# Kernel tuning notes

Measured on AMD Instinct MI355X. Metric: run time of the kernel, lower is better.

The kernel has to match this reference:

```python
import jax, jax.numpy as jnp
import numpy as np

N, DIM, HEADS, DHEAD = 4096, 1024, 16, 64
INNER = HEADS * DHEAD


def setup_inputs() -> dict:
    key = jax.random.key(0)
    ks = jax.random.split(key, 6)
    s_in = 1.0 / np.sqrt(DIM)
    s_inner = 1.0 / np.sqrt(INNER)
    return {
        "x": jax.random.normal(ks[0], (N, DIM), dtype=jnp.float32),
        # weights stored as (in, out) so y = x @ W
        "Wq": jax.random.uniform(ks[1], (DIM, INNER), jnp.float32, -s_in, s_in),
        "Wk": jax.random.uniform(ks[2], (DIM, INNER), jnp.float32, -s_in, s_in),
        "Wv": jax.random.uniform(ks[3], (DIM, INNER), jnp.float32, -s_in, s_in),
        "Wo": jax.random.uniform(ks[4], (INNER, DIM), jnp.float32, -s_inner, s_inner),
        "bo": jax.random.uniform(ks[5], (DIM,), jnp.float32, -s_inner, s_inner),
    }


def reference(x, Wq, Wk, Wv, Wo, bo):
    scale = DHEAD ** -0.5
    # [n, h, d] -> [h, n, d]
    q = (x @ Wq).reshape(N, HEADS, DHEAD).transpose(1, 0, 2)
    k = (x @ Wk).reshape(N, HEADS, DHEAD).transpose(1, 0, 2)
    v = (x @ Wv).reshape(N, HEADS, DHEAD).transpose(1, 0, 2)
    dots = jnp.einsum("hnd,hmd->hnm", q, k) * scale  # [h, n, n]
    attn = jax.nn.softmax(dots, axis=-1)
    out = jnp.einsum("hnm,hmd->hnd", attn, v)  # [h, n, d]
    out = out.transpose(1, 0, 2).reshape(N, INNER)
    return out @ Wo + bo
```

## Files before the change

### kernel.cpp

```cpp
#include <hip/hip_runtime.h>
#include <cstdint>
#include <cstddef>

typedef _Float16 f16;
typedef _Float16 f16x8 __attribute__((ext_vector_type(8)));
typedef _Float16 f16x4 __attribute__((ext_vector_type(4)));
typedef __fp16 fp16x2 __attribute__((ext_vector_type(2)));
typedef float floatx4 __attribute__((ext_vector_type(4)));
typedef float floatx16 __attribute__((ext_vector_type(16)));

constexpr int SEQ = 4096;
constexpr int DIM = 1024;
constexpr int NHEAD = 16;
constexpr int DH = 64;

#define QSCALE 0.18033688011112042f

__device__ __forceinline__ void async16(void* lds, const void* g) {
  __builtin_amdgcn_global_load_lds(
      (__attribute__((address_space(1))) void*)g,
      (__attribute__((address_space(3))) void*)lds, 16, 0, 0);
}

__device__ __forceinline__ uint32_t pk2(float a, float b) {
  union { fp16x2 h; uint32_t u; } c;
  c.h = __builtin_amdgcn_cvt_pkrtz(a, b);
  return c.u;
}

__device__ __forceinline__ float dot2acc(uint32_t packed, float acc) {
#if __has_builtin(__builtin_amdgcn_fdot2)
  union { uint32_t u; fp16x2 h; } c; c.u = packed;
  fp16x2 one2; one2.x = (__fp16)1.0f; one2.y = (__fp16)1.0f;
  return __builtin_amdgcn_fdot2(c.h, one2, acc, false);
#else
  union { uint32_t u; fp16x2 h; } c; c.u = packed;
  return acc + (float)c.h.x + (float)c.h.y;
#endif
}


__global__ void cvt_x(const float* __restrict__ x, f16* __restrict__ xh) {
  int i = (blockIdx.x * 256 + threadIdx.x) * 4;
  float4 v = *(const float4*)(x + i);
  f16x4 o;
  o.x = (f16)v.x; o.y = (f16)v.y; o.z = (f16)v.z; o.w = (f16)v.w;
  *(f16x4*)(xh + i) = o;
}

__global__ void transpose_cvt(const float* __restrict__ w0, const float* __restrict__ w1,
                              const float* __restrict__ w2, const float* __restrict__ w3,
                              f16* __restrict__ o0, f16* __restrict__ o1,
                              f16* __restrict__ o2, f16* __restrict__ o3) {
  __shared__ float tile[32][33];
  int z = blockIdx.z;
  const float* W = (z == 0) ? w0 : (z == 1) ? w1 : (z == 2) ? w2 : w3;
  f16* O = (z == 0) ? o0 : (z == 1) ? o1 : (z == 2) ? o2 : o3;
  int tx = threadIdx.x, ty = threadIdx.y;
  int xc = blockIdx.x * 32 + tx;
  for (int i = ty; i < 32; i += 8)
    tile[i][tx] = W[(size_t)(blockIdx.y * 32 + i) * DIM + xc];
  __syncthreads();
  int xo = blockIdx.y * 32 + tx;
  for (int i = ty; i < 32; i += 8)
    O[(size_t)(blockIdx.x * 32 + i) * DIM + xo] = (f16)tile[tx][i];
}

__global__ __launch_bounds__(256, 3) void gemm_qkv(
    const f16* __restrict__ xh, const f16* __restrict__ wqt,
    const f16* __restrict__ wkt, const f16* __restrict__ wvt,
    f16* __restrict__ q_ws, f16* __restrict__ k_ws, f16* __restrict__ vt_ws) {
  __shared__ f16 smem[16896];
  f16* a_lds = smem;
  f16* b_lds = smem + 4096;
  const int tid = threadIdx.x;
  const int lane = tid & 63, l16 = lane & 15, quad = lane >> 4;
  const int w = tid >> 6, wr = w >> 1, wc = w & 1;
  const int m0 = blockIdx.x * 128, n0 = blockIdx.y * 128;
  const int z = blockIdx.z;
  const f16* Bt = (z == 0) ? wqt : (z == 1) ? wkt : wvt;

  floatx4 acc[4][4];
#pragma unroll
  for (int mt = 0; mt < 4; ++mt)
#pragma unroll
    for (int nt = 0; nt < 4; ++nt) acc[mt][nt] = (floatx4){0.f, 0.f, 0.f, 0.f};

  for (int k0 = 0; k0 < DIM; k0 += 32) {
#pragma unroll
    for (int rnd = 0; rnd < 2; ++rnd) {
      int e = (rnd * 256 + tid) * 8;
      int cb = e >> 10, r = (e >> 3) & 127;
      async16(a_lds + e, xh + (size_t)(m0 + r) * DIM + k0 + cb * 8);
      async16(b_lds + e, Bt + (size_t)(n0 + r) * DIM + k0 + cb * 8);
    }
    __syncthreads();
    f16x8 af[4], bq[4];
#pragma unroll
    for (int mt = 0; mt < 4; ++mt)
      af[mt] = *(const f16x8*)(a_lds + quad * 1024 + (wr * 64 + mt * 16 + l16) * 8);
#pragma unroll
    for (int nt = 0; nt < 4; ++nt)
      bq[nt] = *(const f16x8*)(b_lds + quad * 1024 + (wc * 64 + nt * 16 + l16) * 8);
#pragma unroll
    for (int mt = 0; mt < 4; ++mt)
#pragma unroll
      for (int nt = 0; nt < 4; ++nt)
        acc[mt][nt] = __builtin_amdgcn_mfma_f32_16x16x32_f16(af[mt], bq[nt], acc[mt][nt], 0, 0, 0);
    __syncthreads();
  }

  if (z < 2) {
#pragma unroll
    for (int mt = 0; mt < 4; ++mt)
#pragma unroll
      for (int nt = 0; nt < 4; ++nt)
#pragma unroll
        for (int r = 0; r < 4; ++r) {
          int m = m0 + wr * 64 + mt * 16 + quad * 4 + r;
          int c = n0 + wc * 64 + nt * 16 + l16;
          float v = acc[mt][nt][r];
          if (z == 0)
            q_ws[(size_t)((c >> 6) * SEQ + m) * DH + (c & 63)] = (f16)(v * QSCALE);
          else
            k_ws[(size_t)((c >> 6) * SEQ + m) * DH + (c & 63)] = (f16)v;
        }
  } else {
#pragma unroll
    for (int mt = 0; mt < 4; ++mt)
#pragma unroll
      for (int nt = 0; nt < 4; ++nt)
#pragma unroll
        for (int r = 0; r < 4; ++r) {
          int cl = wc * 64 + nt * 16 + l16;
          int ml = wr * 64 + mt * 16 + quad * 4 + r;
          smem[cl * 132 + ml] = (f16)acc[mt][nt][r];
        }
    __syncthreads();
#pragma unroll
    for (int it = 0; it < 8; ++it) {
      int idx = it * 256 + tid;
      int cl = idx >> 4, mp = (idx & 15) * 8;
      f16x4 lo = *(const f16x4*)(smem + cl * 132 + mp);
      f16x4 hi4 = *(const f16x4*)(smem + cl * 132 + mp + 4);
      f16x8 v8;
#pragma unroll
      for (int j = 0; j < 4; ++j) { v8[j] = lo[j]; v8[4 + j] = hi4[j]; }
      *(f16x8*)(vt_ws + (size_t)(n0 + cl) * SEQ + m0 + mp) = v8;
    }
  }
}

__global__ __launch_bounds__(256, 4) void attn_kernel(
    const f16* __restrict__ qg, const f16* __restrict__ kg,
    const f16* __restrict__ vtg, f16* __restrict__ po, float* __restrict__ ps) {
  __shared__ f16 smem[16384];
  f16* k_lds = smem;
  f16* v_lds = smem + 8192;

  const int tid = threadIdx.x;
  const int w = tid >> 6, lane = tid & 63, l32 = lane & 31;
  const int hi = lane >> 5;
  const int h = blockIdx.y, qt = blockIdx.x, half = blockIdx.z;
  const int q0 = qt * 128 + w * 32;

  f16x8 qf[4];
#pragma unroll
  for (int kf = 0; kf < 4; ++kf)
    qf[kf] = *(const f16x8*)(qg + (size_t)(h * SEQ + q0 + l32) * DH + kf * 16 + hi * 8);

  floatx16 oacc[2];
  oacc[0] = (floatx16)0.f; oacc[1] = (floatx16)0.f;
  float ssum = 0.f;

  const int kt0 = half * (SEQ / 256), kt1 = kt0 + (SEQ / 256);
  for (int kt = kt0; kt < kt1; ++kt) {
#pragma unroll
    for (int rnd = 0; rnd < 4; ++rnd) {
      int e = (rnd * 256 + tid) * 8;
      {
        int cb = e >> 10, r = (e >> 3) & 127;
        async16(k_lds + e, kg + (size_t)(h * SEQ + kt * 128 + r) * DH + cb * 8);
      }
      {
        int cb = e >> 9, r = (e >> 3) & 63;
        async16(v_lds + e, vtg + (size_t)(h * DH + r) * SEQ + kt * 128 + cb * 8);
      }
    }
    __syncthreads();

#pragma unroll
    for (int kb = 0; kb < 4; ++kb) {
      floatx16 sacc = (floatx16)0.f;
#pragma unroll
      for (int kf = 0; kf < 4; ++kf) {
        f16x8 kfrag = *(const f16x8*)(k_lds + (kf * 2 + hi) * 1024 + (kb * 32 + l32) * 8);
        sacc = __builtin_amdgcn_mfma_f32_32x32x16_f16(kfrag, qf[kf], sacc, 0, 0, 0);
      }
      float p[16];
#pragma unroll
      for (int r = 0; r < 16; ++r) p[r] = exp2f(sacc[r]);
#pragma unroll
      for (int kh = 0; kh < 2; ++kh) {
        uint32_t d0a = pk2(p[8 * kh + 0], p[8 * kh + 1]);
        uint32_t d0b = pk2(p[8 * kh + 2], p[8 * kh + 3]);
        uint32_t d1a = pk2(p[8 * kh + 4], p[8 * kh + 5]);
        uint32_t d1b = pk2(p[8 * kh + 6], p[8 * kh + 7]);
        ssum = dot2acc(d0a, ssum);
        ssum = dot2acc(d0b, ssum);
        ssum = dot2acc(d1a, ssum);
        ssum = dot2acc(d1b, ssum);
        uint32_t ra = (uint32_t)__shfl_xor((int)(hi ? d0a : d1a), 32);
        uint32_t rb = (uint32_t)__shfl_xor((int)(hi ? d0b : d1b), 32);
        union { uint32_t u[4]; f16x8 v; } bu;
        bu.u[0] = hi ? ra : d0a;
        bu.u[1] = hi ? rb : d0b;
        bu.u[2] = hi ? d1a : ra;
        bu.u[3] = hi ? d1b : rb;
        f16x8 bfrag = bu.v;
        int cb = kb * 4 + kh * 2 + hi;
#pragma unroll
        for (int dt = 0; dt < 2; ++dt) {
          f16x8 vfrag = *(const f16x8*)(v_lds + cb * 512 + (dt * 32 + l32) * 8);
          oacc[dt] = __builtin_amdgcn_mfma_f32_32x32x16_f16(vfrag, bfrag, oacc[dt], 0, 0, 0);
        }
      }
    }
    __syncthreads();
  }

  ssum += __shfl_xor(ssum, 32);
  const int tileid = (half * NHEAD + h) * 32 + qt;
  if (hi == 0) ps[(size_t)tileid * 128 + w * 32 + l32] = ssum;

  f16* pob = po + (size_t)tileid * 8192;
#pragma unroll
  for (int dt = 0; dt < 2; ++dt)
#pragma unroll
    for (int r = 0; r < 16; ++r) {
      int d = dt * 32 + (r & 3) + 8 * (r >> 2) + 4 * hi;
      pob[d * 128 + w * 32 + l32] = (f16)oacc[dt][r];
    }
}

__global__ __launch_bounds__(256, 4) void combine(
    const f16* __restrict__ po, const float* __restrict__ ps, f16* __restrict__ og) {
  __shared__ float inv_s[128];
  __shared__ f16 t[128 * 68];
  const int tid = threadIdx.x;
  const int h = blockIdx.y, qt = blockIdx.x;
  const int t0 = h * 32 + qt, t1 = (NHEAD + h) * 32 + qt;
  if (tid < 128) inv_s[tid] = 1.f / (ps[(size_t)t0 * 128 + tid] + ps[(size_t)t1 * 128 + tid]);
  __syncthreads();
  const f16* b0 = po + (size_t)t0 * 8192;
  const f16* b1 = po + (size_t)t1 * 8192;
#pragma unroll
  for (int it = 0; it < 4; ++it) {
    int e = (it * 256 + tid) * 8;
    int d = e >> 7, q = e & 127;
    f16x8 a = *(const f16x8*)(b0 + e);
    f16x8 b = *(const f16x8*)(b1 + e);
#pragma unroll
    for (int j = 0; j < 8; ++j)
      t[(q + j) * 68 + d] = (f16)(((float)a[j] + (float)b[j]) * inv_s[q + j]);
  }
  __syncthreads();
#pragma unroll
  for (int it = 0; it < 4; ++it) {
    int idx = it * 256 + tid;
    int q = idx >> 3, dcol = (idx & 7) * 8;
    f16x4 lo = *(const f16x4*)(t + q * 68 + dcol);
    f16x4 hi4 = *(const f16x4*)(t + q * 68 + dcol + 4);
    f16x8 v8;
#pragma unroll
    for (int j = 0; j < 4; ++j) { v8[j] = lo[j]; v8[4 + j] = hi4[j]; }
    *(f16x8*)(og + (size_t)(qt * 128 + q) * DIM + h * DH + dcol) = v8;
  }
}

__global__ __launch_bounds__(256, 2) void gemm_o(
    const f16* __restrict__ ab, const f16* __restrict__ wot,
    const float* __restrict__ bo, float* __restrict__ out) {
  __shared__ f16 a_lds[4096];
  __shared__ f16 b_lds[2048];
  const int tid = threadIdx.x;
  const int lane = tid & 63, l16 = lane & 15, quad = lane >> 4;
  const int w = tid >> 6, wr = w >> 1, wc = w & 1;
  const int m0 = blockIdx.x * 128, n0 = blockIdx.y * 64;

  floatx4 acc[4][2];
#pragma unroll
  for (int mt = 0; mt < 4; ++mt)
#pragma unroll
    for (int nt = 0; nt < 2; ++nt) acc[mt][nt] = (floatx4){0.f, 0.f, 0.f, 0.f};

  for (int k0 = 0; k0 < DIM; k0 += 32) {
#pragma unroll
    for (int rnd = 0; rnd < 2; ++rnd) {
      int e = (rnd * 256 + tid) * 8;
      int cb = e >> 10, r = (e >> 3) & 127;
      async16(a_lds + e, ab + (size_t)(m0 + r) * DIM + k0 + cb * 8);
    }
    {
      int e = tid * 8;
      int cb = e >> 9, r = (e >> 3) & 63;
      async16(b_lds + e, wot + (size_t)(n0 + r) * DIM + k0 + cb * 8);
    }
    __syncthreads();
    f16x8 af[4], bq[2];
#pragma unroll
    for (int mt = 0; mt < 4; ++mt)
      af[mt] = *(const f16x8*)(a_lds + quad * 1024 + (wr * 64 + mt * 16 + l16) * 8);
#pragma unroll
    for (int nt = 0; nt < 2; ++nt)
      bq[nt] = *(const f16x8*)(b_lds + quad * 512 + (wc * 32 + nt * 16 + l16) * 8);
#pragma unroll
    for (int mt = 0; mt < 4; ++mt)
#pragma unroll
      for (int nt = 0; nt < 2; ++nt)
        acc[mt][nt] = __builtin_amdgcn_mfma_f32_16x16x32_f16(af[mt], bq[nt], acc[mt][nt], 0, 0, 0);
    __syncthreads();
  }

#pragma unroll
  for (int mt = 0; mt < 4; ++mt)
#pragma unroll
    for (int nt = 0; nt < 2; ++nt)
#pragma unroll
      for (int r = 0; r < 4; ++r) {
        int m = m0 + wr * 64 + mt * 16 + quad * 4 + r;
        int c = n0 + wc * 32 + nt * 16 + l16;
        out[(size_t)m * DIM + c] = acc[mt][nt][r] + bo[c];
      }
}


extern "C" void kernel_launch(void* const* d_in, const int* in_sizes, int n_in,
                              void* d_out, int out_size, void* d_ws, size_t ws_size,
                              hipStream_t stream) {
  (void)in_sizes; (void)n_in; (void)out_size; (void)ws_size;
  const float* x  = (const float*)d_in[0];
  const float* Wq = (const float*)d_in[1];
  const float* Wk = (const float*)d_in[2];
  const float* Wv = (const float*)d_in[3];
  const float* Wo = (const float*)d_in[4];
  const float* bo = (const float*)d_in[5];
  float* out = (float*)d_out;
  char* ws = (char*)d_ws;

  f16* xh    = (f16*)(ws);
  f16* wqt   = (f16*)(ws + (8u  << 20));
  f16* wkt   = (f16*)(ws + (10u << 20));
  f16* wvt   = (f16*)(ws + (12u << 20));
  f16* wot   = (f16*)(ws + (14u << 20));
  f16* q_ws  = (f16*)(ws + (16u << 20));
  f16* k_ws  = (f16*)(ws + (24u << 20));
  f16* vt_ws = (f16*)(ws + (32u << 20));
  f16* po    = (f16*)(ws + (40u << 20));
  float* ps  = (float*)(ws + (57u << 20));
  f16* aout  = xh;

  cvt_x<<<dim3(SEQ * DIM / 1024), dim3(256), 0, stream>>>(x, xh);
  transpose_cvt<<<dim3(32, 32, 4), dim3(32, 8), 0, stream>>>(Wq, Wk, Wv, Wo, wqt, wkt, wvt, wot);
  gemm_qkv<<<dim3(32, 8, 3), dim3(256), 0, stream>>>(xh, wqt, wkt, wvt, q_ws, k_ws, vt_ws);
  attn_kernel<<<dim3(SEQ / 128, NHEAD, 2), dim3(256), 0, stream>>>(q_ws, k_ws, vt_ws, po, ps);
  combine<<<dim3(SEQ / 128, NHEAD), dim3(256), 0, stream>>>(po, ps, aout);
  gemm_o<<<dim3(32, 16), dim3(256), 0, stream>>>(aout, wot, bo, out);
}
```

Measured before the change: 292.1 us.

## Double-buffer K/V tiles in attention with async prefetch and permlane swap

The attention loop now uses a two-stage LDS ping-pong with 64-key tiles. The next tile's K and V^T are prefetched via async global-to-LDS loads while the current tile is computed, and the kernel waits with explicit vmcnt counts and raw s_barrier instead of __syncthreads. It also replaces the cross-half shuffle with permlane32_swap when available and raises wave priority around MFMA groups. The goal is to hide global load latency behind compute, at the cost of more barriers per key (smaller tiles) and a hand-written waitcnt that must match the issue count.

```diff
diff --git a/kernel.cpp b/kernel.cpp
--- a/kernel.cpp
+++ b/kernel.cpp
@@ -155,8 +155,6 @@
     const f16* __restrict__ qg, const f16* __restrict__ kg,
     const f16* __restrict__ vtg, f16* __restrict__ po, float* __restrict__ ps) {
   __shared__ f16 smem[16384];
-  f16* k_lds = smem;
-  f16* v_lds = smem + 8192;
 
   const int tid = threadIdx.x;
   const int w = tid >> 6, lane = tid & 63, l32 = lane & 31;
@@ -173,30 +171,54 @@
   oacc[0] = (floatx16)0.f; oacc[1] = (floatx16)0.f;
   float ssum = 0.f;
 
-  const int kt0 = half * (SEQ / 256), kt1 = kt0 + (SEQ / 256);
-  for (int kt = kt0; kt < kt1; ++kt) {
-#pragma unroll
-    for (int rnd = 0; rnd < 4; ++rnd) {
+  const f16* kg_h = kg + (size_t)h * SEQ * DH;
+  const f16* vt_h = vtg + (size_t)h * DH * SEQ;
+  const int kb0 = half * (SEQ / 128);
+  constexpr int NT = SEQ / 128;
+
+  {
+    const f16* ks = kg_h + (size_t)(kb0 * 64) * DH;
+    const f16* vs = vt_h + kb0 * 64;
+#pragma unroll
+    for (int rnd = 0; rnd < 2; ++rnd) {
       int e = (rnd * 256 + tid) * 8;
-      {
-        int cb = e >> 10, r = (e >> 3) & 127;
-        async16(k_lds + e, kg + (size_t)(h * SEQ + kt * 128 + r) * DH + cb * 8);
+      int cb = e >> 9, r = (e >> 3) & 63;
+      async16(smem + e, ks + (size_t)r * DH + cb * 8);
+      async16(smem + 4096 + e, vs + (size_t)r * SEQ + cb * 8);
+    }
+  }
+
+  for (int i = 0; i < NT; ++i) {
+    f16* k_lds = smem + (i & 1) * 8192;
+    f16* v_lds = k_lds + 4096;
+    if (i + 1 < NT) {
+      f16* kn = smem + ((i + 1) & 1) * 8192;
+      const f16* ks = kg_h + (size_t)((kb0 + i + 1) * 64) * DH;
+      const f16* vs = vt_h + (kb0 + i + 1) * 64;
+#pragma unroll
+      for (int rnd = 0; rnd < 2; ++rnd) {
+        int e = (rnd * 256 + tid) * 8;
+        int cb = e >> 9, r = (e >> 3) & 63;
+        async16(kn + e, ks + (size_t)r * DH + cb * 8);
+        async16(kn + 4096 + e, vs + (size_t)r * SEQ + cb * 8);
       }
-      {
-        int cb = e >> 9, r = (e >> 3) & 63;
-        async16(v_lds + e, vtg + (size_t)(h * DH + r) * SEQ + kt * 128 + cb * 8);
-      }
-    }
-    __syncthreads();
-
-#pragma unroll
-    for (int kb = 0; kb < 4; ++kb) {
+      asm volatile("s_waitcnt vmcnt(4)" ::: "memory");
+    } else {
+      asm volatile("s_waitcnt vmcnt(0)" ::: "memory");
+    }
+    __builtin_amdgcn_s_barrier();
+    asm volatile("" ::: "memory");
+
+#pragma unroll
+    for (int kb = 0; kb < 2; ++kb) {
       floatx16 sacc = (floatx16)0.f;
+      __builtin_amdgcn_s_setprio(1);
 #pragma unroll
       for (int kf = 0; kf < 4; ++kf) {
-        f16x8 kfrag = *(const f16x8*)(k_lds + (kf * 2 + hi) * 1024 + (kb * 32 + l32) * 8);
+        f16x8 kfrag = *(const f16x8*)(k_lds + (kf * 2 + hi) * 512 + (kb * 32 + l32) * 8);
         sacc = __builtin_amdgcn_mfma_f32_32x32x16_f16(kfrag, qf[kf], sacc, 0, 0, 0);
       }
+      __builtin_amdgcn_s_setprio(0);
       float p[16];
 #pragma unroll
       for (int r = 0; r < 16; ++r) p[r] = exp2f(sacc[r]);
@@ -210,23 +232,36 @@
         ssum = dot2acc(d0b, ssum);
         ssum = dot2acc(d1a, ssum);
         ssum = dot2acc(d1b, ssum);
-        uint32_t ra = (uint32_t)__shfl_xor((int)(hi ? d0a : d1a), 32);
-        uint32_t rb = (uint32_t)__shfl_xor((int)(hi ? d0b : d1b), 32);
         union { uint32_t u[4]; f16x8 v; } bu;
-        bu.u[0] = hi ? ra : d0a;
-        bu.u[1] = hi ? rb : d0b;
-        bu.u[2] = hi ? d1a : ra;
-        bu.u[3] = hi ? d1b : rb;
-        f16x8 bfrag = bu.v;
+#if __has_builtin(__builtin_amdgcn_permlane32_swap)
+        {
+          auto s1 = __builtin_amdgcn_permlane32_swap(d0a, d1a, false, false);
+          auto s2 = __builtin_amdgcn_permlane32_swap(d0b, d1b, false, false);
+          bu.u[0] = s1[0]; bu.u[1] = s2[0]; bu.u[2] = s1[1]; bu.u[3] = s2[1];
+        }
+#else
+        {
+          uint32_t ra = (uint32_t)__shfl_xor((int)(hi ? d0a : d1a), 32);
+          uint32_t rb = (uint32_t)__shfl_xor((int)(hi ? d0b : d1b), 32);
+          bu.u[0] = hi ? ra : d0a;
+          bu.u[1] = hi ? rb : d0b;
+          bu.u[2] = hi ? d1a : ra;
+          bu.u[3] = hi ? d1b : rb;
+        }
+#endif
         int cb = kb * 4 + kh * 2 + hi;
+        __builtin_amdgcn_s_setprio(1);
 #pragma unroll
         for (int dt = 0; dt < 2; ++dt) {
           f16x8 vfrag = *(const f16x8*)(v_lds + cb * 512 + (dt * 32 + l32) * 8);
-          oacc[dt] = __builtin_amdgcn_mfma_f32_32x32x16_f16(vfrag, bfrag, oacc[dt], 0, 0, 0);
+          oacc[dt] = __builtin_amdgcn_mfma_f32_32x32x16_f16(vfrag, bu.v, oacc[dt], 0, 0, 0);
         }
+        __builtin_amdgcn_s_setprio(0);
       }
     }
-    __syncthreads();
+    asm volatile("" ::: "memory");
+    __builtin_amdgcn_s_barrier();
+    asm volatile("" ::: "memory");
   }
 
   ssum += __shfl_xor(ssum, 32);
```

Measured after the change: 279.5 us. 4.3% less time.
